# Optimization experiments

Hardware: AMD Instinct MI355X
Metric: run time of the kernel (lower is better)

## Reference

```python
import jax, jax.numpy as jnp
import numpy as np

HQ, HKV, DK, DV = 8, 4, 128, 128
WIDTH, CLIP, MAXPOS = 16, 5.0, 2048
EPS = 1e-5

def rms_bn(x, g, ch_axis):
    # EMA_RMSBatchNorm (eval with batch stats): per-channel RMS over all other dims
    axes = tuple(i for i in range(x.ndim) if i != ch_axis)
    ms = jnp.mean(jnp.square(x), axis=axes, keepdims=True)
    shape = [1] * x.ndim; shape[ch_axis] = g.shape[0]
    return x * jax.lax.rsqrt(ms + EPS) * g.reshape(shape)

def ln(x, g, b):
    m = jnp.mean(x, -1, keepdims=True)
    v = jnp.mean(jnp.square(x - m), -1, keepdims=True)
    return (x - m) * jax.lax.rsqrt(v + EPS) * g + b

def rope(x):
    # x: [B,S,H,C], custom AlphaGenome frequency schedule
    B, S, H, C = x.shape
    nf = C // 2
    pos = jnp.arange(S, dtype=x.dtype)
    lin = jnp.arange(nf, dtype=x.dtype)
    end = max(MAXPOS - nf + 1.0, 1.0)
    geom = jnp.exp(jnp.linspace(0.0, np.log(end), nf).astype(x.dtype))
    inv_freq = 1.0 / (lin + geom)
    theta = jnp.repeat(pos[:, None] * inv_freq, 2, axis=-1)[None, :, None, :]  # [1,S,1,C]
    x_rot = jnp.stack([-x[..., 1::2], x[..., ::2]], axis=-1).reshape(x.shape)
    return x * jnp.cos(theta) + x_rot * jnp.sin(theta)

def _forward(x, pair_x, ab_bn_g, ab_fc_w, bn1_g, wq, wk, wv, qn_g, qn_b, kn_g, kn_b,
             vn_g, vn_b, wo, bo, bn2_g, mbn1_g, w1, b1, w2, b2, mbn2_g):
    B, S, C = x.shape
    # --- AttentionBias from pair representation ---
    pb = rms_bn(pair_x, ab_bn_g, 3)
    pb = jax.nn.gelu(pb, approximate=False)
    pb = jnp.einsum('bijc,gc->bijg', pb, ab_fc_w)          # [B,Sp,Sp,group]
    pb = jnp.repeat(jnp.repeat(pb, WIDTH, axis=1), WIDTH, axis=2)  # upsample to [B,S,S,group]
    bias = jnp.repeat(jnp.transpose(pb, (0, 3, 1, 2)), HKV, axis=1)  # [B,HQ,S,S]
    # --- GQA attention ---
    xn = rms_bn(x, bn1_g, 2)
    q = ln((xn @ wq.T).reshape(B, S, HQ, DK), qn_g, qn_b)
    k = ln((xn @ wk.T).reshape(B, S, HKV, DK), kn_g, kn_b)
    v = ln((xn @ wv.T).reshape(B, S, HKV, DV), vn_g, vn_b)
    q = rope(q); k = rope(k)
    rep = HQ // HKV
    k = jnp.tile(k, (1, 1, rep, 1))  # torch .repeat: [k0..k3, k0..k3]
    v = jnp.tile(v, (1, 1, rep, 1))
    logits = jnp.einsum('bshd,bThd->bhsT', q, k) / np.float32(np.sqrt(DK)) + bias
    logits = jnp.tanh(logits / CLIP) * CLIP
    attn = jax.nn.softmax(logits, axis=-1)
    y = jnp.einsum('bhsT,bThd->bshd', attn, v)
    # faithful to original: permute then reshape (layout scramble preserved)
    y = jnp.transpose(y, (0, 2, 1, 3)).reshape(B, S, HQ * DV)
    x = x + rms_bn(y @ wo.T + bo, bn2_g, 2)
    # --- MLP block ---
    h = jax.nn.relu(rms_bn(x, mbn1_g, 2) @ w1.T + b1)
    x = x + rms_bn(h @ w2.T + b2, mbn2_g, 2)
    return x, pair_x

def setup_inputs() -> dict:
    key = jax.random.key(0)
    ks = jax.random.split(key, 10)
    B, S, C, SP, PC = 2, 2048, 768, 128, 128
    n = lambda k, sh: jax.random.normal(k, sh, jnp.float32) * 0.02
    d = {}
    d['x'] = jax.random.normal(ks[0], (B, S, C), jnp.float32)
    d['pair_x'] = jax.random.normal(ks[1], (B, SP, SP, PC), jnp.float32)
    d['ab_bn_g'] = jnp.ones((PC,), jnp.float32)
    d['ab_fc_w'] = n(ks[2], (HQ // HKV, PC))
    d['bn1_g'] = jnp.ones((C,), jnp.float32)
    d['wq'] = n(ks[3], (HQ * DK, C))
    d['wk'] = n(ks[4], (HKV * DK, C))
    d['wv'] = n(ks[5], (HKV * DV, C))
    d['qn_g'] = jnp.ones((DK,), jnp.float32); d['qn_b'] = jnp.zeros((DK,), jnp.float32)
    d['kn_g'] = jnp.ones((DK,), jnp.float32); d['kn_b'] = jnp.zeros((DK,), jnp.float32)
    d['vn_g'] = jnp.ones((DV,), jnp.float32); d['vn_b'] = jnp.zeros((DV,), jnp.float32)
    d['wo'] = n(ks[6], (C, HQ * DV)); d['bo'] = jnp.zeros((C,), jnp.float32)
    d['bn2_g'] = jnp.ones((C,), jnp.float32)
    d['mbn1_g'] = jnp.ones((C,), jnp.float32)
    d['w1'] = n(ks[7], (2 * C, C)); d['b1'] = jnp.zeros((2 * C,), jnp.float32)
    d['w2'] = n(ks[8], (C, 2 * C)); d['b2'] = jnp.zeros((C,), jnp.float32)
    d['mbn2_g'] = jnp.ones((C,), jnp.float32)
    return d

def reference(x, pair_x, ab_bn_g, ab_fc_w, bn1_g, wq, wk, wv, qn_g, qn_b, kn_g, kn_b,
              vn_g, vn_b, wo, bo, bn2_g, mbn1_g, w1, b1, w2, b2, mbn2_g):
    return _forward(x, pair_x, ab_bn_g, ab_fc_w, bn1_g, wq, wk, wv, qn_g, qn_b, kn_g,
                    kn_b, vn_g, vn_b, wo, bo, bn2_g, mbn1_g, w1, b1, w2, b2, mbn2_g)
```

## Files before the change

### kernel.cpp

```cpp
#include <hip/hip_runtime.h>
#include <math.h>

#define EPS 1e-5f

typedef __attribute__((ext_vector_type(8))) short short8;
typedef __attribute__((ext_vector_type(4))) float f32x4;

namespace {

constexpr int Bn = 2, Sn = 2048, Cn = 768;
constexpr float INV_BS = 1.0f / 4096.0f;
constexpr float INV_PAIR = 1.0f / 32768.0f;
constexpr float LOG2E = 1.4426950408889634f;

__device__ __forceinline__ ushort f2bf(float f) {
  uint u = __float_as_uint(f);
  u = (u + 0x7fffu + ((u >> 16) & 1u)) >> 16;
  return (ushort)u;
}
__device__ __forceinline__ float bf2f(ushort u) {
  return __uint_as_float(((uint)u) << 16);
}
__device__ __forceinline__ uint cvt_pk_bf16(float lo, float hi) {
  uint r;
  asm("v_cvt_pk_bf16_f32 %0, %1, %2" : "=v"(r) : "v"(lo), "v"(hi));
  return r;
}
__device__ __forceinline__ void gl16(const ushort* g, ushort* l) {
  __builtin_amdgcn_global_load_lds(
      (const __attribute__((address_space(1))) unsigned int*)(unsigned long long)(size_t)g,
      (__attribute__((address_space(3))) unsigned int*)(unsigned int)(size_t)l, 16, 0, 0);
}

#define KSW(r, c) ((((r) * 128) + (c)) ^ (((r) & 7) * 8))
#define VTW(d, t) ((((d) * 64) + (t)) ^ (((d) & 7) * 8))
#define PSW2(w, q, c) ((w) * 2048 + ((((q) * 64) + (c)) ^ (((q) & 7) * 8)))

__global__ __launch_bounds__(256) void prep_k(
    const float* __restrict__ wq, const float* __restrict__ wk,
    const float* __restrict__ wv, const float* __restrict__ wo,
    const float* __restrict__ w1, const float* __restrict__ w2,
    ushort* __restrict__ wdst, float2* __restrict__ rtab,
    const float* __restrict__ pair, float* __restrict__ ps,
    const float* __restrict__ x, float* __restrict__ xs) {
  const int blk = blockIdx.x;
  const int tid = threadIdx.x;
  if (blk < 2304) {
    int u = blk * 256 + tid;
    const float* src; int local;
    if (u < 98304)       { src = wq; local = u; }
    else if (u < 147456) { src = wk; local = u - 98304; }
    else if (u < 196608) { src = wv; local = u - 147456; }
    else if (u < 294912) { src = wo; local = u - 196608; }
    else if (u < 442368) { src = w1; local = u - 294912; }
    else                 { src = w2; local = u - 442368; }
    int i = local * 8;
    float4 a = *(const float4*)&src[i];
    float4 b = *(const float4*)&src[i + 4];
    union { short8 s8; ushort us[8]; } o;
    o.us[0] = f2bf(a.x); o.us[1] = f2bf(a.y); o.us[2] = f2bf(a.z); o.us[3] = f2bf(a.w);
    o.us[4] = f2bf(b.x); o.us[5] = f2bf(b.y); o.us[6] = f2bf(b.z); o.us[7] = f2bf(b.w);
    *(short8*)&wdst[u * 8] = o.s8;
  } else if (blk < 2816) {
    int idx = (blk - 2304) * 256 + tid;
    int s = idx >> 6, i = idx & 63;
    const float kGeo = logf(1985.0f) * (1.0f / 63.0f);
    float inv = 1.0f / ((float)i + expf((float)i * kGeo));
    float th = (float)s * inv;
    rtab[idx] = make_float2(cosf(th), sinf(th));
  } else if (blk < 2944) {
    int c = tid & 127;
    int r0 = (blk - 2816) * 256 + (tid >> 7) * 128;
    float acc = 0.f;
    for (int r = 0; r < 128; ++r) {
      float v = pair[(size_t)(r0 + r) * 128 + c];
      acc += v * v;
    }
    atomicAdd(&ps[c], acc);
  } else {
    int r0 = (blk - 2944) * 16;
    float a0 = 0.f, a1 = 0.f, a2 = 0.f;
    for (int r = 0; r < 16; ++r) {
      const float* row = x + (size_t)(r0 + r) * 768;
      float v0 = row[tid], v1 = row[tid + 256], v2 = row[tid + 512];
      a0 += v0 * v0; a1 += v1 * v1; a2 += v2 * v2;
    }
    atomicAdd(&xs[tid], a0);
    atomicAdd(&xs[tid + 256], a1);
    atomicAdd(&xs[tid + 512], a2);
  }
}

__global__ void scale_cast_k(const float* __restrict__ a, const float* __restrict__ sums,
                             const float* __restrict__ g, ushort* __restrict__ o) {
  int idx = blockIdx.x * 256 + threadIdx.x;
  int c0 = (idx % 96) * 8;
  int base = idx * 8;
  float4 v0 = *(const float4*)&a[base];
  float4 v1 = *(const float4*)&a[base + 4];
  union { short8 s8; ushort us[8]; } r;
  float vv[8] = {v0.x, v0.y, v0.z, v0.w, v1.x, v1.y, v1.z, v1.w};
#pragma unroll
  for (int j = 0; j < 8; ++j) {
    float sc = rsqrtf(sums[c0 + j] * INV_BS + EPS) * g[c0 + j];
    r.us[j] = f2bf(vv[j] * sc);
  }
  *(short8*)&o[base] = r.s8;
}

__global__ void ch_sumsq768_k(const float* __restrict__ a, float* __restrict__ out) {
  int r0 = blockIdx.x * 16;
  int c = threadIdx.x;
  float acc = 0.f;
  for (int r = 0; r < 16; ++r) {
    float v = a[(size_t)(r0 + r) * 768 + c];
    acc += v * v;
  }
  atomicAdd(&out[c], acc);
}

__global__ __launch_bounds__(256) void pair_bias_k(
    const float* __restrict__ p, const float* __restrict__ ps,
    const float* __restrict__ g, const float* __restrict__ w,
    float* __restrict__ pb2, float* __restrict__ pcopy) {
  const int tid = threadIdx.x;
  const int lane32 = tid & 31;
  const int sub = tid >> 5;
  const int c0 = lane32 * 4;
  float4 gv = *(const float4*)&g[c0];
  float4 psv = *(const float4*)&ps[c0];
  float4 w0 = *(const float4*)&w[c0];
  float4 w1v = *(const float4*)&w[128 + c0];
  float sc[4] = {rsqrtf(psv.x * INV_PAIR + EPS) * gv.x,
                 rsqrtf(psv.y * INV_PAIR + EPS) * gv.y,
                 rsqrtf(psv.z * INV_PAIR + EPS) * gv.z,
                 rsqrtf(psv.w * INV_PAIR + EPS) * gv.w};
  float wa[4] = {w0.x, w0.y, w0.z, w0.w};
  float wb[4] = {w1v.x, w1v.y, w1v.z, w1v.w};
#pragma unroll
  for (int it = 0; it < 4; ++it) {
    int row = blockIdx.x * 32 + it * 8 + sub;
    float4 v = *(const float4*)&p[(size_t)row * 128 + c0];
    *(float4*)&pcopy[(size_t)row * 128 + c0] = v;
    float vv[4] = {v.x, v.y, v.z, v.w};
    float a0 = 0.f, a1 = 0.f;
#pragma unroll
    for (int j = 0; j < 4; ++j) {
      float x = vv[j] * sc[j];
      float ge = 0.5f * x * (1.f + erff(x * 0.70710678118654752f));
      a0 += ge * wa[j];
      a1 += ge * wb[j];
    }
#pragma unroll
    for (int o = 1; o <= 16; o <<= 1) {
      a0 += __shfl_xor(a0, o);
      a1 += __shfl_xor(a1, o);
    }
    if (lane32 == 0) {
      pb2[(size_t)row * 2 + 0] = a0 * (0.4f * LOG2E);
      pb2[(size_t)row * 2 + 1] = a1 * (0.4f * LOG2E);
    }
  }
}

template <bool RELU, bool OUT_BF16>
__global__ __launch_bounds__(256) void gemm_bf16_k(
    const ushort* __restrict__ A, const ushort* __restrict__ B,
    void* __restrict__ Cv, int M, int N, int K,
    const float* __restrict__ bias) {
  __shared__ __align__(16) ushort As[128 * 64];
  __shared__ __align__(16) ushort Bs[128 * 64];
  const int m0 = blockIdx.y * 128, n0 = blockIdx.x * 128;
  const int tid = threadIdx.x;
  const int lane = tid & 63;
  const int wid = tid >> 6;
  const int l15 = lane & 15, l4 = lane >> 4;
  const int wm = (wid >> 1) * 64, wn = (wid & 1) * 64;
  const ushort* asrc[4]; const ushort* bsrc[4];
  ushort* adst[4]; ushort* bdst[4];
#pragma unroll
  for (int u = 0; u < 4; ++u) {
    int ci = u * 256 + tid;
    int r = ci >> 3, s = ci & 7, g = s ^ (r & 7);
    asrc[u] = A + (size_t)(m0 + r) * K + g * 8;
    bsrc[u] = B + (size_t)(n0 + r) * K + g * 8;
    adst[u] = &As[(u * 256 + wid * 64) * 8];
    bdst[u] = &Bs[(u * 256 + wid * 64) * 8];
  }
  f32x4 acc[4][4];
#pragma unroll
  for (int i = 0; i < 4; ++i)
#pragma unroll
    for (int j = 0; j < 4; ++j) acc[i][j] = (f32x4){0.f, 0.f, 0.f, 0.f};
  for (int k0 = 0; k0 < K; k0 += 64) {
#pragma unroll
    for (int u = 0; u < 4; ++u) {
      gl16(asrc[u] + k0, adst[u]);
      gl16(bsrc[u] + k0, bdst[u]);
    }
    __syncthreads();
#pragma unroll
    for (int ks = 0; ks < 2; ++ks) {
      const int sw = ((ks * 4 + l4) ^ (l15 & 7)) * 8;
      short8 af[4], bf[4];
#pragma unroll
      for (int i = 0; i < 4; ++i) af[i] = *(const short8*)&As[(wm + i * 16 + l15) * 64 + sw];
#pragma unroll
      for (int j = 0; j < 4; ++j) bf[j] = *(const short8*)&Bs[(wn + j * 16 + l15) * 64 + sw];
#pragma unroll
      for (int i = 0; i < 4; ++i)
#pragma unroll
        for (int j = 0; j < 4; ++j)
          acc[i][j] = __builtin_amdgcn_mfma_f32_16x16x32_bf16(af[i], bf[j], acc[i][j], 0, 0, 0);
    }
    __syncthreads();
  }
  float* Cf = (float*)Cv;
  ushort* Cb = (ushort*)Cv;
#pragma unroll
  for (int j = 0; j < 4; ++j) {
    int col = n0 + wn + j * 16 + l15;
    float bv = bias ? bias[col] : 0.f;
#pragma unroll
    for (int i = 0; i < 4; ++i) {
      int row = m0 + wm + i * 16 + l4 * 4;
#pragma unroll
      for (int r = 0; r < 4; ++r) {
        float v = acc[i][j][r] + bv;
        if (RELU) v = fmaxf(v, 0.f);
        if (OUT_BF16) Cb[(size_t)(row + r) * N + col] = f2bf(v);
        else Cf[(size_t)(row + r) * N + col] = v;
      }
    }
  }
}

template <bool SUMSQ>
__global__ __launch_bounds__(256) void gemm64_bf16_k(
    const ushort* __restrict__ A, const ushort* __restrict__ B,
    float* __restrict__ Cf, int M, int N, int K,
    const float* __restrict__ bias, float* __restrict__ ssq) {
  __shared__ __align__(16) ushort As[64 * 64];
  __shared__ __align__(16) ushort Bs[128 * 64];
  const int m0 = blockIdx.y * 64, n0 = blockIdx.x * 128;
  const int tid = threadIdx.x;
  const int lane = tid & 63;
  const int wid = tid >> 6;
  const int l15 = lane & 15, l4 = lane >> 4;
  const int wn = wid * 32;
  const ushort* asrc[2]; ushort* adst[2];
  const ushort* bsrc[4]; ushort* bdst[4];
#pragma unroll
  for (int u = 0; u < 2; ++u) {
    int ci = u * 256 + tid;
    int r = ci >> 3, s = ci & 7, g = s ^ (r & 7);
    asrc[u] = A + (size_t)(m0 + r) * K + g * 8;
    adst[u] = &As[(u * 256 + wid * 64) * 8];
  }
#pragma unroll
  for (int u = 0; u < 4; ++u) {
    int ci = u * 256 + tid;
    int r = ci >> 3, s = ci & 7, g = s ^ (r & 7);
    bsrc[u] = B + (size_t)(n0 + r) * K + g * 8;
    bdst[u] = &Bs[(u * 256 + wid * 64) * 8];
  }
  f32x4 acc[4][2];
#pragma unroll
  for (int i = 0; i < 4; ++i)
#pragma unroll
    for (int j = 0; j < 2; ++j) acc[i][j] = (f32x4){0.f, 0.f, 0.f, 0.f};
  for (int k0 = 0; k0 < K; k0 += 64) {
#pragma unroll
    for (int u = 0; u < 2; ++u) gl16(asrc[u] + k0, adst[u]);
#pragma unroll
    for (int u = 0; u < 4; ++u) gl16(bsrc[u] + k0, bdst[u]);
    __syncthreads();
#pragma unroll
    for (int ks = 0; ks < 2; ++ks) {
      const int sw = ((ks * 4 + l4) ^ (l15 & 7)) * 8;
      short8 af[4], bf[2];
#pragma unroll
      for (int i = 0; i < 4; ++i) af[i] = *(const short8*)&As[(i * 16 + l15) * 64 + sw];
#pragma unroll
      for (int j = 0; j < 2; ++j) bf[j] = *(const short8*)&Bs[(wn + j * 16 + l15) * 64 + sw];
#pragma unroll
      for (int i = 0; i < 4; ++i)
#pragma unroll
        for (int j = 0; j < 2; ++j)
          acc[i][j] = __builtin_amdgcn_mfma_f32_16x16x32_bf16(af[i], bf[j], acc[i][j], 0, 0, 0);
    }
    __syncthreads();
  }
#pragma unroll
  for (int j = 0; j < 2; ++j) {
    int col = n0 + wn + j * 16 + l15;
    float bv = bias ? bias[col] : 0.f;
    float sq = 0.f;
#pragma unroll
    for (int i = 0; i < 4; ++i) {
      int row = m0 + i * 16 + l4 * 4;
#pragma unroll
      for (int r = 0; r < 4; ++r) {
        float v = acc[i][j][r] + bv;
        if (SUMSQ) sq += v * v;
        Cf[(size_t)(row + r) * N + col] = v;
      }
    }
    if (SUMSQ) {
      sq += __shfl_xor(sq, 16);
      sq += __shfl_xor(sq, 32);
      if (l4 == 0) atomicAdd(&ssq[col], sq);
    }
  }
}

__global__ __launch_bounds__(256) void ln_rope_k(
    const float* __restrict__ qkv, const float2* __restrict__ rtab,
    const float* __restrict__ qg, const float* __restrict__ qb,
    const float* __restrict__ kg, const float* __restrict__ kb,
    const float* __restrict__ vg, const float* __restrict__ vb,
    ushort* __restrict__ q_b, ushort* __restrict__ k_b, ushort* __restrict__ v_b) {
  const int half = threadIdx.x >> 7;
  const int tid = threadIdx.x & 127;
  const int bs = blockIdx.x * 2 + half;
  const int slot = blockIdx.y;
  const int s = bs & (Sn - 1);
  const int b = bs >> 11;
  const float* src; const float* g; const float* be; ushort* dst; bool dorope; bool isq = false;
  if (slot < 8) {
    src = qkv + (size_t)bs * 2048 + slot * 128;
    g = qg; be = qb;
    dst = q_b + ((size_t)(b * 8 + slot) * Sn + s) * 128;
    dorope = true; isq = true;
  } else if (slot < 12) {
    int h = slot - 8;
    src = qkv + (size_t)bs * 2048 + 1024 + h * 128;
    g = kg; be = kb;
    dst = k_b + ((size_t)(b * 4 + h) * Sn + s) * 128;
    dorope = true;
  } else {
    int h = slot - 12;
    src = qkv + (size_t)bs * 2048 + 1536 + h * 128;
    g = vg; be = vb;
    dst = v_b + ((size_t)(b * 4 + h) * Sn + s) * 128;
    dorope = false;
  }
  __shared__ float sh[2][128];
  __shared__ float red[2][4];
  float v = src[tid];
  float sum = v;
#pragma unroll
  for (int o = 32; o >= 1; o >>= 1) sum += __shfl_xor(sum, o);
  if ((tid & 63) == 0) red[half][tid >> 6] = sum;
  __syncthreads();
  float mean = (red[half][0] + red[half][1]) * (1.f / 128.f);
  float d = v - mean;
  float s2 = d * d;
#pragma unroll
  for (int o = 32; o >= 1; o >>= 1) s2 += __shfl_xor(s2, o);
  if ((tid & 63) == 0) red[half][2 + (tid >> 6)] = s2;
  __syncthreads();
  float var = (red[half][2] + red[half][3]) * (1.f / 128.f);
  float val = d * rsqrtf(var + EPS) * g[tid] + be[tid];
  if (dorope) {
    sh[half][tid] = val;
    __syncthreads();
    float2 cssn = rtab[(s << 6) | (tid >> 1)];
    float rot = (tid & 1) ? sh[half][tid - 1] : -sh[half][tid + 1];
    val = val * cssn.x + rot * cssn.y;
  }
  if (isq) val *= 0.035355339059327376f * LOG2E;
  dst[tid] = f2bf(val);
}

__global__ __launch_bounds__(256) void vtrans_k(const ushort* __restrict__ vb,
                                                ushort* __restrict__ vtt) {
  __shared__ __align__(16) ushort T[64][136];
  const int hv = blockIdx.y, s0 = blockIdx.x * 64;
  const int tid = threadIdx.x;
  const ushort* src = vb + ((size_t)hv * Sn + s0) * 128;
#pragma unroll
  for (int u = 0; u < 4; ++u) {
    int fi = u * 256 + tid;
    int r = fi >> 4, c = (fi & 15) * 8;
    *(float4*)&T[r][c] = *(const float4*)&src[(size_t)r * 128 + c];
  }
  __syncthreads();
  ushort* dst = vtt + (size_t)hv * 128 * Sn + s0;
#pragma unroll
  for (int u = 0; u < 4; ++u) {
    int fi = u * 256 + tid;
    int d = fi >> 3, t8 = (fi & 7) * 8;
    union { float4 f4; ushort us[8]; } o;
#pragma unroll
    for (int j = 0; j < 8; ++j) o.us[j] = T[t8 + j][d];
    *(float4*)&dst[(size_t)d * Sn + t8] = o.f4;
  }
}

__global__ __launch_bounds__(256, 2) void flash_v14_k(
    const ushort* __restrict__ qb, const ushort* __restrict__ kb,
    const ushort* __restrict__ vtt, const float* __restrict__ pb2,
    ushort* __restrict__ part_y, float* __restrict__ part_l) {
  __shared__ __align__(16) ushort Ks[64 * 128];
  __shared__ __align__(16) ushort Vt[128 * 64];
  __shared__ __align__(16) ushort Ps[4 * 32 * 64];
  const int s0 = blockIdx.x * 128;
  const int bh = blockIdx.y;
  const int half = blockIdx.z;
  const int b = bh >> 3, h = bh & 7;
  const int kv = h & 3, grp = h >> 2;
  const int tid = threadIdx.x;
  const int wid = tid >> 6, lane = tid & 63;
  const int l15 = lane & 15, l4 = lane >> 4;
  const ushort* kbase = kb + (size_t)(b * 4 + kv) * Sn * 128;
  const ushort* vbase = vtt + (size_t)(b * 4 + kv) * 128 * Sn;
  const int qr0 = s0 + wid * 32;
  short8 qf[2][4];
#pragma unroll
  for (int rg = 0; rg < 2; ++rg)
#pragma unroll
    for (int kc = 0; kc < 4; ++kc)
      qf[rg][kc] = *(const short8*)&qb[((size_t)bh * Sn + qr0 + rg * 16 + l15) * 128 + kc * 32 + l4 * 8];
  const ushort* ksrc[4]; const ushort* vsrc[4];
  ushort* kdst[4]; ushort* vdst[4];
#pragma unroll
  for (int u = 0; u < 4; ++u) {
    int ci = u * 256 + tid;
    int kr = ci >> 4, kg = (ci & 15) ^ (kr & 7);
    ksrc[u] = kbase + (size_t)kr * 128 + kg * 8;
    kdst[u] = &Ks[(u * 256 + wid * 64) * 8];
    int vd = ci >> 3, vg = (ci & 7) ^ (vd & 7);
    vsrc[u] = vbase + (size_t)vd * Sn + vg * 8;
    vdst[u] = &Vt[(u * 256 + wid * 64) * 8];
  }
  f32x4 y[2][8];
#pragma unroll
  for (int rg = 0; rg < 2; ++rg)
#pragma unroll
    for (int i = 0; i < 8; ++i) y[rg][i] = (f32x4){0.f, 0.f, 0.f, 0.f};
  float lsum[2] = {0.f, 0.f};
  const float C2 = -10.f * LOG2E;
  const int tbeg = half * 1024;
  for (int t0 = tbeg; t0 < tbeg + 1024; t0 += 64) {
    __syncthreads();
#pragma unroll
    for (int u = 0; u < 4; ++u) {
      gl16(ksrc[u] + (size_t)t0 * 128, kdst[u]);
      gl16(vsrc[u] + t0, vdst[u]);
    }
    __syncthreads();
    f32x4 acc[2][4];
#pragma unroll
    for (int rg = 0; rg < 2; ++rg)
#pragma unroll
      for (int nb = 0; nb < 4; ++nb) acc[rg][nb] = (f32x4){0.f, 0.f, 0.f, 0.f};
    __builtin_amdgcn_s_setprio(1);
#pragma unroll
    for (int kc = 0; kc < 4; ++kc)
#pragma unroll
      for (int nb = 0; nb < 4; ++nb) {
        short8 kf = *(const short8*)&Ks[KSW(nb * 16 + l15, kc * 32 + l4 * 8)];
        acc[0][nb] = __builtin_amdgcn_mfma_f32_16x16x32_bf16(kf, qf[0][kc], acc[0][nb], 0, 0, 0);
        acc[1][nb] = __builtin_amdgcn_mfma_f32_16x16x32_bf16(kf, qf[1][kc], acc[1][nb], 0, 0, 0);
      }
    __builtin_amdgcn_s_setprio(0);
#pragma unroll
    for (int rg = 0; rg < 2; ++rg)
#pragma unroll
      for (int nb = 0; nb < 4; ++nb) {
        float bias = pb2[(((size_t)b * 128 + (s0 >> 4) + wid * 2 + rg) * 128 + (t0 >> 4) + nb) * 2 + grp];
        float p[4];
#pragma unroll
        for (int r = 0; r < 4; ++r) {
          float e = exp2f(acc[rg][nb][r] + bias);
          p[r] = exp2f(C2 * __builtin_amdgcn_rcpf(e + 1.f));
        }
        lsum[rg] += (p[0] + p[1]) + (p[2] + p[3]);
        uint2 pk;
        pk.x = cvt_pk_bf16(p[0], p[1]);
        pk.y = cvt_pk_bf16(p[2], p[3]);
        *(uint2*)&Ps[PSW2(wid, rg * 16 + l15, nb * 16 + l4 * 4)] = pk;
      }
    __builtin_amdgcn_s_setprio(1);
#pragma unroll
    for (int ks = 0; ks < 2; ++ks) {
      short8 pa0 = *(const short8*)&Ps[PSW2(wid, l15, ks * 32 + l4 * 8)];
      short8 pa1 = *(const short8*)&Ps[PSW2(wid, 16 + l15, ks * 32 + l4 * 8)];
#pragma unroll
      for (int nbd = 0; nbd < 8; ++nbd) {
        short8 vf = *(const short8*)&Vt[VTW(nbd * 16 + l15, ks * 32 + l4 * 8)];
        y[0][nbd] = __builtin_amdgcn_mfma_f32_16x16x32_bf16(pa0, vf, y[0][nbd], 0, 0, 0);
        y[1][nbd] = __builtin_amdgcn_mfma_f32_16x16x32_bf16(pa1, vf, y[1][nbd], 0, 0, 0);
      }
    }
    __builtin_amdgcn_s_setprio(0);
  }
#pragma unroll
  for (int rg = 0; rg < 2; ++rg) {
    float ls = lsum[rg];
    ls += __shfl_xor(ls, 16);
    ls += __shfl_xor(ls, 32);
    if (l4 == 0) part_l[(size_t)(half * 16 + bh) * Sn + qr0 + rg * 16 + l15] = ls;
    ushort* pybase = part_y + ((size_t)(half * 16 + bh) * Sn + qr0 + rg * 16) * 128;
#pragma unroll
    for (int nbd = 0; nbd < 8; ++nbd)
#pragma unroll
      for (int r = 0; r < 4; ++r)
        pybase[(size_t)(l4 * 4 + r) * 128 + nbd * 16 + l15] = f2bf(y[rg][nbd][r]);
  }
}

__global__ void combine_k(const ushort* __restrict__ part_y, const float* __restrict__ part_l,
                          ushort* __restrict__ attn_b) {
  int t = blockIdx.x * 256 + threadIdx.x;
  int row = t >> 4;
  size_t o0 = (size_t)row * 128 + (t & 15) * 8;
  float acc[8] = {};
#pragma unroll
  for (int hf = 0; hf < 2; ++hf) {
    union { short8 s8; ushort us[8]; } u;
    u.s8 = *(const short8*)&part_y[o0 + (size_t)hf * 4194304];
#pragma unroll
    for (int j = 0; j < 8; ++j) acc[j] += bf2f(u.us[j]);
  }
  float rcp = 1.f / (part_l[row] + part_l[row + 32768]);
  union { short8 s8; ushort us[8]; } o;
#pragma unroll
  for (int j = 0; j < 8; ++j) o.us[j] = f2bf(acc[j] * rcp);
  *(short8*)&attn_b[o0] = o.s8;
}

template <bool SUMSQ>
__global__ void add_scale_k(const float* __restrict__ base, const float* __restrict__ delta,
                            const float* __restrict__ sums, const float* __restrict__ g,
                            float* __restrict__ out, float* __restrict__ ssq) {
  const int c = threadIdx.x;
  const float sc = rsqrtf(sums[c] * INV_BS + EPS) * g[c];
  const int r0 = blockIdx.x * 16;
  float sq = 0.f;
  for (int r = 0; r < 16; ++r) {
    size_t idx = (size_t)(r0 + r) * 768 + c;
    float v = base[idx] + delta[idx] * sc;
    out[idx] = v;
    if (SUMSQ) sq += v * v;
  }
  if (SUMSQ) atomicAdd(&ssq[c], sq);
}

}

extern "C" void kernel_launch(void* const* d_in, const int* in_sizes, int n_in,
                              void* d_out, int out_size, void* d_ws, size_t ws_size,
                              hipStream_t stream) {
  const float* x       = (const float*)d_in[0];
  const float* pair_x  = (const float*)d_in[1];
  const float* ab_bn_g = (const float*)d_in[2];
  const float* ab_fc_w = (const float*)d_in[3];
  const float* bn1_g   = (const float*)d_in[4];
  const float* wq      = (const float*)d_in[5];
  const float* wk      = (const float*)d_in[6];
  const float* wv      = (const float*)d_in[7];
  const float* qn_g    = (const float*)d_in[8];
  const float* qn_b    = (const float*)d_in[9];
  const float* kn_g    = (const float*)d_in[10];
  const float* kn_b    = (const float*)d_in[11];
  const float* vn_g    = (const float*)d_in[12];
  const float* vn_b    = (const float*)d_in[13];
  const float* wo      = (const float*)d_in[14];
  const float* bo      = (const float*)d_in[15];
  const float* bn2_g   = (const float*)d_in[16];
  const float* mbn1_g  = (const float*)d_in[17];
  const float* w1      = (const float*)d_in[18];
  const float* b1      = (const float*)d_in[19];
  const float* w2      = (const float*)d_in[20];
  const float* b2      = (const float*)d_in[21];
  const float* mbn2_g  = (const float*)d_in[22];
  float* out = (float*)d_out;
  float* ws = (float*)d_ws;

  float* ps    = ws + 0;
  float* xs    = ws + 256;
  float* es    = ws + 1024;
  float* x2s   = ws + 2048;
  float* fs    = ws + 3072;
  float* pb2   = ws + 4096;
  ushort* wall_b = (ushort*)(ws + 69632);
  ushort* wo_b = (ushort*)(ws + 856064);
  ushort* w1_b = (ushort*)(ws + 1249280);
  ushort* w2_b = (ushort*)(ws + 1839104);
  ushort* xn_b = (ushort*)(ws + 2428928);
  float* qkvtmp = ws + 4001792;
  ushort* q_b  = (ushort*)(ws + 12390400);
  ushort* k_b  = (ushort*)(ws + 14487552);
  ushort* v_b  = (ushort*)(ws + 15536128);
  float2* rtab = (float2*)(ws + 16584704);
  ushort* v_tt = (ushort*)(ws + 2428928);
  ushort* part_y = (ushort*)(ws + 3477504);
  float* part_l = ws + 11866112;
  ushort* attn_b = (ushort*)(ws + 11997184);
  float* proj  = ws + 3477504;
  float* x2    = ws + 6623232;
  ushort* x2n_b = (ushort*)(ws + 9768960);
  ushort* hbuf_b = (ushort*)(ws + 3477504);
  float* proj2 = ws + 11341824;

  (void)hipMemsetAsync(ws, 0, 4096 * sizeof(float), stream);

  prep_k<<<3200, 256, 0, stream>>>(wq, wk, wv, wo, w1, w2, wall_b, rtab,
                                   pair_x, ps, x, xs);
  pair_bias_k<<<1024, 256, 0, stream>>>(pair_x, ps, ab_bn_g, ab_fc_w, pb2, out + 3145728);
  scale_cast_k<<<1536, 256, 0, stream>>>(x, xs, bn1_g, xn_b);
  gemm_bf16_k<false, false><<<dim3(16, 32), 256, 0, stream>>>(xn_b, wall_b, qkvtmp, 4096, 2048, 768, nullptr);
  ln_rope_k<<<dim3(2048, 16), 256, 0, stream>>>(qkvtmp, rtab, qn_g, qn_b, kn_g, kn_b,
                                                vn_g, vn_b, q_b, k_b, v_b);
  vtrans_k<<<dim3(32, 8), 256, 0, stream>>>(v_b, v_tt);
  flash_v14_k<<<dim3(16, 16, 2), 256, 0, stream>>>(q_b, k_b, v_tt, pb2, part_y, part_l);
  combine_k<<<2048, 256, 0, stream>>>(part_y, part_l, attn_b);
  gemm64_bf16_k<true><<<dim3(6, 64), 256, 0, stream>>>(attn_b, wo_b, proj, 4096, 768, 1024, bo, es);
  add_scale_k<true><<<256, 768, 0, stream>>>(x, proj, es, bn2_g, x2, x2s);
  scale_cast_k<<<1536, 256, 0, stream>>>(x2, x2s, mbn1_g, x2n_b);
  gemm_bf16_k<true, true><<<dim3(12, 32), 256, 0, stream>>>(x2n_b, w1_b, hbuf_b, 4096, 1536, 768, b1);
  gemm64_bf16_k<true><<<dim3(6, 64), 256, 0, stream>>>(hbuf_b, w2_b, proj2, 4096, 768, 1536, b2, fs);
  add_scale_k<false><<<256, 768, 0, stream>>>(x2, proj2, fs, mbn2_g, out, nullptr);
}
```

Before: 254.0 us.

## Fuse QKV GEMM with LayerNorm, RoPE and V transpose epilogue

Replaces the QKV GEMM, separate LayerNorm+RoPE kernel and V transpose kernel with a single GEMM whose epilogue computes per-head LN statistics via shuffles and shared memory, applies RoPE using lane-pair shuffles, and writes bf16 q/k and transposed v directly. This removes the fp32 qkv intermediate round trip (about 32MB written and read) and two kernel launches. Variance is now computed as E[x^2]-mean^2 in one pass, a small numerical change, and the epilogue's stores are scattered 2-byte writes for q/k.

```diff
diff --git a/kernel.cpp b/kernel.cpp
--- a/kernel.cpp
+++ b/kernel.cpp
@@ -108,17 +108,6 @@
   *(short8*)&o[base] = r.s8;
 }
 
-__global__ void ch_sumsq768_k(const float* __restrict__ a, float* __restrict__ out) {
-  int r0 = blockIdx.x * 16;
-  int c = threadIdx.x;
-  float acc = 0.f;
-  for (int r = 0; r < 16; ++r) {
-    float v = a[(size_t)(r0 + r) * 768 + c];
-    acc += v * v;
-  }
-  atomicAdd(&out[c], acc);
-}
-
 __global__ __launch_bounds__(256) void pair_bias_k(
     const float* __restrict__ p, const float* __restrict__ ps,
     const float* __restrict__ g, const float* __restrict__ w,
@@ -163,6 +152,143 @@
   }
 }
 
+__global__ __launch_bounds__(256) void gemm_qkv_k(
+    const ushort* __restrict__ A, const ushort* __restrict__ B, int K,
+    const float* __restrict__ qn_g, const float* __restrict__ qn_b,
+    const float* __restrict__ kn_g, const float* __restrict__ kn_b,
+    const float* __restrict__ vn_g, const float* __restrict__ vn_b,
+    const float2* __restrict__ rtab,
+    ushort* __restrict__ q_b, ushort* __restrict__ k_b, ushort* __restrict__ v_tt) {
+  __shared__ __align__(16) ushort As[128 * 64];
+  __shared__ __align__(16) ushort Bs[128 * 64];
+  __shared__ float2 redS[128][2];
+  const int m0 = blockIdx.y * 128, n0 = blockIdx.x * 128;
+  const int tid = threadIdx.x;
+  const int lane = tid & 63;
+  const int wid = tid >> 6;
+  const int l15 = lane & 15, l4 = lane >> 4;
+  const int wm = (wid >> 1) * 64, wn = (wid & 1) * 64;
+  const ushort* asrc[4]; const ushort* bsrc[4];
+  ushort* adst[4]; ushort* bdst[4];
+#pragma unroll
+  for (int u = 0; u < 4; ++u) {
+    int ci = u * 256 + tid;
+    int r = ci >> 3, s = ci & 7, g = s ^ (r & 7);
+    asrc[u] = A + (size_t)(m0 + r) * K + g * 8;
+    bsrc[u] = B + (size_t)(n0 + r) * K + g * 8;
+    adst[u] = &As[(u * 256 + wid * 64) * 8];
+    bdst[u] = &Bs[(u * 256 + wid * 64) * 8];
+  }
+  f32x4 acc[4][4];
+#pragma unroll
+  for (int i = 0; i < 4; ++i)
+#pragma unroll
+    for (int j = 0; j < 4; ++j) acc[i][j] = (f32x4){0.f, 0.f, 0.f, 0.f};
+  for (int k0 = 0; k0 < K; k0 += 64) {
+#pragma unroll
+    for (int u = 0; u < 4; ++u) {
+      gl16(asrc[u] + k0, adst[u]);
+      gl16(bsrc[u] + k0, bdst[u]);
+    }
+    __syncthreads();
+#pragma unroll
+    for (int ks = 0; ks < 2; ++ks) {
+      const int sw = ((ks * 4 + l4) ^ (l15 & 7)) * 8;
+      short8 af[4], bf[4];
+#pragma unroll
+      for (int i = 0; i < 4; ++i) af[i] = *(const short8*)&As[(wm + i * 16 + l15) * 64 + sw];
+#pragma unroll
+      for (int j = 0; j < 4; ++j) bf[j] = *(const short8*)&Bs[(wn + j * 16 + l15) * 64 + sw];
+#pragma unroll
+      for (int i = 0; i < 4; ++i)
+#pragma unroll
+        for (int j = 0; j < 4; ++j)
+          acc[i][j] = __builtin_amdgcn_mfma_f32_16x16x32_bf16(af[i], bf[j], acc[i][j], 0, 0, 0);
+    }
+    __syncthreads();
+  }
+  const int slot = blockIdx.x;
+  const float* gvec; const float* bvec; int mode;
+  if (slot < 8)       { gvec = qn_g; bvec = qn_b; mode = 0; }
+  else if (slot < 12) { gvec = kn_g; bvec = kn_b; mode = 1; }
+  else                { gvec = vn_g; bvec = vn_b; mode = 2; }
+  float rsum[4][4], rsq[4][4];
+#pragma unroll
+  for (int i = 0; i < 4; ++i)
+#pragma unroll
+    for (int r = 0; r < 4; ++r) {
+      float s1 = 0.f, s2 = 0.f;
+#pragma unroll
+      for (int j = 0; j < 4; ++j) {
+        float a = acc[i][j][r];
+        s1 += a; s2 += a * a;
+      }
+#pragma unroll
+      for (int o = 1; o <= 8; o <<= 1) {
+        s1 += __shfl_xor(s1, o);
+        s2 += __shfl_xor(s2, o);
+      }
+      rsum[i][r] = s1; rsq[i][r] = s2;
+    }
+  if (l15 == 0) {
+#pragma unroll
+    for (int i = 0; i < 4; ++i)
+#pragma unroll
+      for (int r = 0; r < 4; ++r)
+        redS[wm + i * 16 + l4 * 4 + r][wn >> 6] = make_float2(rsum[i][r], rsq[i][r]);
+  }
+  __syncthreads();
+  float gv4[4], bv4[4];
+#pragma unroll
+  for (int j = 0; j < 4; ++j) {
+    int c = wn + j * 16 + l15;
+    gv4[j] = gvec[c]; bv4[j] = bvec[c];
+  }
+  const float QS = 0.035355339059327376f * LOG2E;
+#pragma unroll
+  for (int i = 0; i < 4; ++i) {
+    float mean[4], rstd[4];
+#pragma unroll
+    for (int r = 0; r < 4; ++r) {
+      int row = wm + i * 16 + l4 * 4 + r;
+      float2 h0 = redS[row][0], h1 = redS[row][1];
+      float m = (h0.x + h1.x) * (1.f / 128.f);
+      float v = (h0.y + h1.y) * (1.f / 128.f) - m * m;
+      mean[r] = m; rstd[r] = rsqrtf(v + EPS);
+    }
+    const int row0 = wm + i * 16 + l4 * 4;
+    const int bs0 = m0 + row0;
+    const int s0v = bs0 & (Sn - 1);
+    const int bb = bs0 >> 11;
+#pragma unroll
+    for (int j = 0; j < 4; ++j) {
+      int c = wn + j * 16 + l15;
+      union { unsigned long long u64; ushort us[4]; } pk;
+#pragma unroll
+      for (int r = 0; r < 4; ++r) {
+        float val = (acc[i][j][r] - mean[r]) * rstd[r] * gv4[j] + bv4[j];
+        if (mode < 2) {
+          float sx = __shfl_xor(val, 1);
+          float rot = (c & 1) ? sx : -sx;
+          float2 cssn = rtab[((s0v + r) << 6) | (c >> 1)];
+          val = val * cssn.x + rot * cssn.y;
+          if (mode == 0) {
+            val *= QS;
+            q_b[((size_t)(bb * 8 + slot) * Sn + s0v + r) * 128 + c] = f2bf(val);
+          } else {
+            k_b[((size_t)(bb * 4 + slot - 8) * Sn + s0v + r) * 128 + c] = f2bf(val);
+          }
+        } else {
+          pk.us[r] = f2bf(val);
+        }
+      }
+      if (mode == 2) {
+        *(unsigned long long*)&v_tt[((size_t)(bb * 4 + slot - 12) * 128 + c) * Sn + s0v] = pk.u64;
+      }
+    }
+  }
+}
+
 template <bool RELU, bool OUT_BF16>
 __global__ __launch_bounds__(256) void gemm_bf16_k(
     const ushort* __restrict__ A, const ushort* __restrict__ B,
@@ -311,90 +437,6 @@
       sq += __shfl_xor(sq, 32);
       if (l4 == 0) atomicAdd(&ssq[col], sq);
     }
-  }
-}
-
-__global__ __launch_bounds__(256) void ln_rope_k(
-    const float* __restrict__ qkv, const float2* __restrict__ rtab,
-    const float* __restrict__ qg, const float* __restrict__ qb,
-    const float* __restrict__ kg, const float* __restrict__ kb,
-    const float* __restrict__ vg, const float* __restrict__ vb,
-    ushort* __restrict__ q_b, ushort* __restrict__ k_b, ushort* __restrict__ v_b) {
-  const int half = threadIdx.x >> 7;
-  const int tid = threadIdx.x & 127;
-  const int bs = blockIdx.x * 2 + half;
-  const int slot = blockIdx.y;
-  const int s = bs & (Sn - 1);
-  const int b = bs >> 11;
-  const float* src; const float* g; const float* be; ushort* dst; bool dorope; bool isq = false;
-  if (slot < 8) {
-    src = qkv + (size_t)bs * 2048 + slot * 128;
-    g = qg; be = qb;
-    dst = q_b + ((size_t)(b * 8 + slot) * Sn + s) * 128;
-    dorope = true; isq = true;
-  } else if (slot < 12) {
-    int h = slot - 8;
-    src = qkv + (size_t)bs * 2048 + 1024 + h * 128;
-    g = kg; be = kb;
-    dst = k_b + ((size_t)(b * 4 + h) * Sn + s) * 128;
-    dorope = true;
-  } else {
-    int h = slot - 12;
-    src = qkv + (size_t)bs * 2048 + 1536 + h * 128;
-    g = vg; be = vb;
-    dst = v_b + ((size_t)(b * 4 + h) * Sn + s) * 128;
-    dorope = false;
-  }
-  __shared__ float sh[2][128];
-  __shared__ float red[2][4];
-  float v = src[tid];
-  float sum = v;
-#pragma unroll
-  for (int o = 32; o >= 1; o >>= 1) sum += __shfl_xor(sum, o);
-  if ((tid & 63) == 0) red[half][tid >> 6] = sum;
-  __syncthreads();
-  float mean = (red[half][0] + red[half][1]) * (1.f / 128.f);
-  float d = v - mean;
-  float s2 = d * d;
-#pragma unroll
-  for (int o = 32; o >= 1; o >>= 1) s2 += __shfl_xor(s2, o);
-  if ((tid & 63) == 0) red[half][2 + (tid >> 6)] = s2;
-  __syncthreads();
-  float var = (red[half][2] + red[half][3]) * (1.f / 128.f);
-  float val = d * rsqrtf(var + EPS) * g[tid] + be[tid];
-  if (dorope) {
-    sh[half][tid] = val;
-    __syncthreads();
-    float2 cssn = rtab[(s << 6) | (tid >> 1)];
-    float rot = (tid & 1) ? sh[half][tid - 1] : -sh[half][tid + 1];
-    val = val * cssn.x + rot * cssn.y;
-  }
-  if (isq) val *= 0.035355339059327376f * LOG2E;
-  dst[tid] = f2bf(val);
-}
-
-__global__ __launch_bounds__(256) void vtrans_k(const ushort* __restrict__ vb,
-                                                ushort* __restrict__ vtt) {
-  __shared__ __align__(16) ushort T[64][136];
-  const int hv = blockIdx.y, s0 = blockIdx.x * 64;
-  const int tid = threadIdx.x;
-  const ushort* src = vb + ((size_t)hv * Sn + s0) * 128;
-#pragma unroll
-  for (int u = 0; u < 4; ++u) {
-    int fi = u * 256 + tid;
-    int r = fi >> 4, c = (fi & 15) * 8;
-    *(float4*)&T[r][c] = *(const float4*)&src[(size_t)r * 128 + c];
-  }
-  __syncthreads();
-  ushort* dst = vtt + (size_t)hv * 128 * Sn + s0;
-#pragma unroll
-  for (int u = 0; u < 4; ++u) {
-    int fi = u * 256 + tid;
-    int d = fi >> 3, t8 = (fi & 7) * 8;
-    union { float4 f4; ushort us[8]; } o;
-#pragma unroll
-    for (int j = 0; j < 8; ++j) o.us[j] = T[t8 + j][d];
-    *(float4*)&dst[(size_t)d * Sn + t8] = o.f4;
   }
 }
 
@@ -590,12 +632,10 @@
   ushort* w1_b = (ushort*)(ws + 1249280);
   ushort* w2_b = (ushort*)(ws + 1839104);
   ushort* xn_b = (ushort*)(ws + 2428928);
-  float* qkvtmp = ws + 4001792;
   ushort* q_b  = (ushort*)(ws + 12390400);
   ushort* k_b  = (ushort*)(ws + 14487552);
-  ushort* v_b  = (ushort*)(ws + 15536128);
+  ushort* v_tt = (ushort*)(ws + 7671808);
   float2* rtab = (float2*)(ws + 16584704);
-  ushort* v_tt = (ushort*)(ws + 2428928);
   ushort* part_y = (ushort*)(ws + 3477504);
   float* part_l = ws + 11866112;
   ushort* attn_b = (ushort*)(ws + 11997184);
@@ -611,10 +651,9 @@
                                    pair_x, ps, x, xs);
   pair_bias_k<<<1024, 256, 0, stream>>>(pair_x, ps, ab_bn_g, ab_fc_w, pb2, out + 3145728);
   scale_cast_k<<<1536, 256, 0, stream>>>(x, xs, bn1_g, xn_b);
-  gemm_bf16_k<false, false><<<dim3(16, 32), 256, 0, stream>>>(xn_b, wall_b, qkvtmp, 4096, 2048, 768, nullptr);
-  ln_rope_k<<<dim3(2048, 16), 256, 0, stream>>>(qkvtmp, rtab, qn_g, qn_b, kn_g, kn_b,
-                                                vn_g, vn_b, q_b, k_b, v_b);
-  vtrans_k<<<dim3(32, 8), 256, 0, stream>>>(v_b, v_tt);
+  gemm_qkv_k<<<dim3(16, 32), 256, 0, stream>>>(xn_b, wall_b, 768,
+                                               qn_g, qn_b, kn_g, kn_b, vn_g, vn_b,
+                                               rtab, q_b, k_b, v_tt);
   flash_v14_k<<<dim3(16, 16, 2), 256, 0, stream>>>(q_b, k_b, v_tt, pb2, part_y, part_l);
   combine_k<<<2048, 256, 0, stream>>>(part_y, part_l, attn_b);
   gemm64_bf16_k<true><<<dim3(6, 64), 256, 0, stream>>>(attn_b, wo_b, proj, 4096, 768, 1024, bo, es);
```

After: 239.6 us. 5.7% less time.
